# Optimization experiments

Measured on AMD Instinct MI355X. Metric: run time of the kernel, lower is better.

## Reference

```python
import jax, jax.numpy as jnp
import numpy as np

BN_EPS = 1e-3  # keras BatchNormalization default


def setup_inputs() -> dict:
    key = jax.random.key(0)
    ks = jax.random.split(key, 8)
    B, T, H, W, C = 2, 8, 28, 28, 256
    Ci = 128
    s_in = 1.0 / np.sqrt(C)
    s_ci = 1.0 / np.sqrt(Ci)
    return {
        "x": jax.random.normal(ks[0], (B, T, H, W, C), dtype=jnp.float32),
        "Wg": jax.random.normal(ks[1], (C, Ci), dtype=jnp.float32) * s_in,
        "bg": jnp.zeros((Ci,), dtype=jnp.float32),
        "Wt": jax.random.normal(ks[2], (C, Ci), dtype=jnp.float32) * s_in,
        "bt": jnp.zeros((Ci,), dtype=jnp.float32),
        "Wp": jax.random.normal(ks[3], (C, Ci), dtype=jnp.float32) * s_in,
        "bp": jnp.zeros((Ci,), dtype=jnp.float32),
        "Wo": jax.random.normal(ks[4], (Ci, C), dtype=jnp.float32) * s_ci,
        "bo": jnp.zeros((C,), dtype=jnp.float32),
        "gamma": jnp.ones((C,), dtype=jnp.float32),
        "beta": jnp.zeros((C,), dtype=jnp.float32),
        "moving_mean": jnp.zeros((C,), dtype=jnp.float32),
        "moving_var": jnp.ones((C,), dtype=jnp.float32),
    }


def reference(x, Wg, bg, Wt, bt, Wp, bp, Wo, bo, gamma, beta, moving_mean, moving_var):
    B, T, H, W, C = x.shape
    Ci = Wg.shape[1]
    N = T * H * W
    xf = x.reshape(B, N, C)  # flatten spatial-temporal positions
    # 1x1x1 convs are per-position channel GEMMs
    g_x = xf @ Wg + bg        # [B, N, Ci]
    theta_x = xf @ Wt + bt    # [B, N, Ci]
    phi_x = xf @ Wp + bp      # [B, N, Ci]
    # f = softmax(theta @ phi^T) -- unscaled single-head global attention
    f = jnp.einsum('bnc,bmc->bnm', theta_x, phi_x)  # [B, N, N]
    f = jax.nn.softmax(f, axis=-1)
    y = jnp.einsum('bnm,bmc->bnc', f, g_x)           # [B, N, Ci]
    # conv_out (1x1x1) back to C channels
    y = y @ Wo + bo                                   # [B, N, C]
    # BatchNorm, inference mode (training=None -> moving statistics)
    y = gamma * (y - moving_mean) * jax.lax.rsqrt(moving_var + BN_EPS) + beta
    return x + y.reshape(B, T, H, W, C)
```

## Files before the change

kernel.cpp:

```cpp
#include <hip/hip_runtime.h>

#define BB 2
#define NN 6272
#define CC 256
#define CI 128
#define SEG 7
#define KVSEG (NN / SEG)
#define NIT (KVSEG / 32)
#define LOG2E 1.44269504088896f
#define THR 12.0f

typedef _Float16 f16;
typedef __attribute__((ext_vector_type(2))) __fp16 fp16v2;
typedef __attribute__((ext_vector_type(8))) _Float16 f16x8;
typedef __attribute__((ext_vector_type(4))) float f32x4;

__global__ __launch_bounds__(256) void prep_kernel(
    const float* __restrict__ Wg, const float* __restrict__ Wt, const float* __restrict__ Wp,
    const float* __restrict__ Wo, const float* __restrict__ bg, const float* __restrict__ bt,
    const float* __restrict__ bp, const float* __restrict__ bo,
    const float* __restrict__ gamma, const float* __restrict__ beta,
    const float* __restrict__ mmean, const float* __restrict__ mvar,
    f16* __restrict__ WallT, f16* __restrict__ WoT,
    float* __restrict__ ball, float* __restrict__ bnsc, float* __restrict__ bnsh)
{
    const int idx = blockIdx.x * 256 + threadIdx.x;
    if (idx < 384*256) {
        const int j = idx >> 8, k = idx & 255;
        float v;
        if (j < 128)      v = Wg[k*CI + j];
        else if (j < 256) v = Wt[k*CI + (j-128)] * LOG2E;
        else              v = Wp[k*CI + (j-256)];
        WallT[j*256 + k] = (f16)v;
    } else if (idx < 384*256 + 256*128) {
        const int i2 = idx - 384*256;
        const int ci = i2 >> 7, k = i2 & 127;
        WoT[ci*CI + k] = (f16)Wo[k*CC + ci];
    } else {
        const int i3 = idx - (384*256 + 256*128);
        if (i3 < 384) {
            float v;
            if (i3 < 128)      v = bg[i3];
            else if (i3 < 256) v = bt[i3-128] * LOG2E;
            else               v = bp[i3-256];
            ball[i3] = v;
        } else if (i3 < 640) {
            const int c = i3 - 384;
            bnsc[c] = gamma[c] * rsqrtf(mvar[c] + 1e-3f);
        } else if (i3 < 896) {
            const int c = i3 - 640;
            float sc = gamma[c] * rsqrtf(mvar[c] + 1e-3f);
            bnsh[c] = beta[c] + sc * (bo[c] - mmean[c]);
        }
    }
}

__global__ __launch_bounds__(256) void proj_gemm(
    const float* __restrict__ x, const f16* __restrict__ WallT, const float* __restrict__ ball,
    f16* __restrict__ th, f16* __restrict__ ph, f16* __restrict__ gT)
{
    __shared__ __align__(16) f16 xls[32*264];
    __shared__ __align__(16) f16 gls[128*40];

    const int tid = threadIdx.x;
    const int wid = tid >> 6, lane = tid & 63;
    const int l15 = lane & 15, lg = lane >> 4;
    const int p0 = blockIdx.x * 32;

    {
        const int row = tid >> 3, c0 = (tid & 7) * 32;
        const float* xsrc = x + (size_t)(p0 + row) * CC + c0;
        f16 buf[32];
        #pragma unroll
        for (int i = 0; i < 8; ++i) {
            float4 v = *reinterpret_cast<const float4*>(xsrc + 4*i);
            buf[4*i+0]=(f16)v.x; buf[4*i+1]=(f16)v.y; buf[4*i+2]=(f16)v.z; buf[4*i+3]=(f16)v.w;
        }
        #pragma unroll
        for (int i = 0; i < 4; ++i)
            *reinterpret_cast<f16x8*>(&xls[row*264 + c0 + 8*i]) =
                *reinterpret_cast<f16x8*>(&buf[8*i]);
    }
    __syncthreads();

    f32x4 acc[2][6];
    #pragma unroll
    for (int pt = 0; pt < 2; ++pt)
        #pragma unroll
        for (int t = 0; t < 6; ++t) acc[pt][t] = (f32x4){0.f,0.f,0.f,0.f};

    const f16* wbase = WallT + (size_t)(wid*96 + l15)*256 + lg*8;
    for (int kk = 0; kk < 8; ++kk) {
        f16x8 a0 = *reinterpret_cast<const f16x8*>(&xls[l15*264 + kk*32 + lg*8]);
        f16x8 a1 = *reinterpret_cast<const f16x8*>(&xls[(16 + l15)*264 + kk*32 + lg*8]);
        #pragma unroll
        for (int t = 0; t < 6; ++t) {
            f16x8 bfr = *reinterpret_cast<const f16x8*>(wbase + (size_t)t*16*256 + kk*32);
            acc[0][t] = __builtin_amdgcn_mfma_f32_16x16x32_f16(a0, bfr, acc[0][t], 0, 0, 0);
            acc[1][t] = __builtin_amdgcn_mfma_f32_16x16x32_f16(a1, bfr, acc[1][t], 0, 0, 0);
        }
    }

    const int bidx = (p0 >= NN) ? 1 : 0;
    const int n0 = p0 - bidx * NN;

    #pragma unroll
    for (int t = 0; t < 6; ++t) {
        const int j0 = wid*96 + t*16;
        const float bv = ball[j0 + l15];
        if (j0 < 128) {
            #pragma unroll
            for (int pt = 0; pt < 2; ++pt)
                #pragma unroll
                for (int r = 0; r < 4; ++r)
                    gls[(j0 + l15)*40 + pt*16 + lg*4 + r] = (f16)(acc[pt][t][r] + bv);
        } else if (j0 < 256) {
            #pragma unroll
            for (int pt = 0; pt < 2; ++pt) {
                f16* dst = th + (size_t)(p0 + pt*16 + lg*4)*CI + (j0 - 128) + l15;
                #pragma unroll
                for (int r = 0; r < 4; ++r)
                    dst[(size_t)r*CI] = (f16)(acc[pt][t][r] + bv);
            }
        } else {
            #pragma unroll
            for (int pt = 0; pt < 2; ++pt) {
                f16* dst = ph + (size_t)(p0 + pt*16 + lg*4)*CI + (j0 - 256) + l15;
                #pragma unroll
                for (int r = 0; r < 4; ++r)
                    dst[(size_t)r*CI] = (f16)(acc[pt][t][r] + bv);
            }
        }
    }
    __syncthreads();
    {
        const int ci = tid >> 1, half = tid & 1;
        f16x8 v0 = *reinterpret_cast<const f16x8*>(&gls[ci*40 + half*16]);
        f16x8 v1 = *reinterpret_cast<const f16x8*>(&gls[ci*40 + half*16 + 8]);
        f16* gdst = gT + ((size_t)bidx*(NN/32) + (n0 >> 5))*(CI*32) + ci*32 + half*16;
        *reinterpret_cast<f16x8*>(gdst)     = v0;
        *reinterpret_cast<f16x8*>(gdst + 8) = v1;
    }
}

__global__ __launch_bounds__(256, 3) void attn_kernel(
    const f16* __restrict__ th, const f16* __restrict__ ph,
    const f16* __restrict__ gT, f16* __restrict__ pacc, float* __restrict__ pml)
{
    __shared__ __align__(16) f16 ph_lds[32 * 128];
    __shared__ __align__(16) f16 g_lds[128 * 32];
    __shared__ __align__(16) f16 pT_lds[4][2][16][40];

    const int b   = blockIdx.z;
    const int seg = blockIdx.y;
    const int tid = threadIdx.x;
    const int wid = tid >> 6;
    const int lane = tid & 63;
    const int l15 = lane & 15;
    const int lg  = lane >> 4;
    const int qw  = blockIdx.x * 128 + wid * 32;

    const f16* thb = th + (size_t)b * NN * CI;
    const f16* phb = ph + (size_t)b * NN * CI;
    const f16* gTb = gT + (size_t)b * (NN/32) * (CI*32);

    f16x8 bf[2][4];
    #pragma unroll
    for (int qt = 0; qt < 2; ++qt) {
        const f16* trow = thb + (size_t)(qw + qt*16 + l15) * CI + lg * 8;
        #pragma unroll
        for (int kk = 0; kk < 4; ++kk)
            bf[qt][kk] = *reinterpret_cast<const f16x8*>(trow + kk * 32);
    }

    f32x4 acc[2][8];
    f32x4 accl[2];
    float m[2] = {-INFINITY, -INFINITY};
    #pragma unroll
    for (int qt = 0; qt < 2; ++qt) {
        #pragma unroll
        for (int ct = 0; ct < 8; ++ct) acc[qt][ct] = (f32x4){0.f,0.f,0.f,0.f};
        accl[qt] = (f32x4){0.f,0.f,0.f,0.f};
    }

    const f16x8 onesA = {(f16)1,(f16)1,(f16)1,(f16)1,(f16)1,(f16)1,(f16)1,(f16)1};

    const int prow = tid >> 3, pcol = (tid & 7) * 16;
    const int pswz = (prow & 7) << 3;
    const int pc0 = pcol ^ pswz, pc1 = (pcol + 8) ^ pswz;
    const int grow = tid >> 1, gcs = (tid & 1) * 16;
    const int gswz = ((grow >> 1) & 3) << 3;
    const int gc0 = gcs ^ gswz, gc1 = (gcs + 8) ^ gswz;

    const int kv_base = seg * KVSEG;
    const int t0 = kv_base >> 5;
    const int xsw = (l15 & 7) << 3;

    #pragma unroll 1
    for (int it = 0; it < NIT; ++it) {
        const int kv0 = kv_base + it * 32;

        const f16* ps = phb + (size_t)(kv0 + prow) * CI + pcol;
        f16x8 pv0 = *reinterpret_cast<const f16x8*>(ps);
        f16x8 pv1 = *reinterpret_cast<const f16x8*>(ps + 8);
        const f16* gs = gTb + (size_t)(t0 + it) * (CI*32) + tid * 16;
        f16x8 gv0 = *reinterpret_cast<const f16x8*>(gs);
        f16x8 gv1 = *reinterpret_cast<const f16x8*>(gs + 8);

        __syncthreads();
        *reinterpret_cast<f16x8*>(&ph_lds[prow*128 + pc0]) = pv0;
        *reinterpret_cast<f16x8*>(&ph_lds[prow*128 + pc1]) = pv1;
        *reinterpret_cast<f16x8*>(&g_lds[grow*32 + gc0])   = gv0;
        *reinterpret_cast<f16x8*>(&g_lds[grow*32 + gc1])   = gv1;
        __syncthreads();

        f32x4 s00 = (f32x4){0.f,0.f,0.f,0.f}, s01 = (f32x4){0.f,0.f,0.f,0.f};
        f32x4 s10 = (f32x4){0.f,0.f,0.f,0.f}, s11 = (f32x4){0.f,0.f,0.f,0.f};
        #pragma unroll
        for (int kk = 0; kk < 4; ++kk) {
            const int coff = (kk*32 + lg*8) ^ xsw;
            f16x8 a0 = *reinterpret_cast<const f16x8*>(&ph_lds[l15*128 + coff]);
            f16x8 a1 = *reinterpret_cast<const f16x8*>(&ph_lds[(16 + l15)*128 + coff]);
            s00 = __builtin_amdgcn_mfma_f32_16x16x32_f16(a0, bf[0][kk], s00, 0, 0, 0);
            s01 = __builtin_amdgcn_mfma_f32_16x16x32_f16(a1, bf[0][kk], s01, 0, 0, 0);
            s10 = __builtin_amdgcn_mfma_f32_16x16x32_f16(a0, bf[1][kk], s10, 0, 0, 0);
            s11 = __builtin_amdgcn_mfma_f32_16x16x32_f16(a1, bf[1][kk], s11, 0, 0, 0);
        }

        float tm0 = fmaxf(fmaxf(fmaxf(s00[0], s00[1]), fmaxf(s00[2], s00[3])),
                          fmaxf(fmaxf(s01[0], s01[1]), fmaxf(s01[2], s01[3])));
        float tm1 = fmaxf(fmaxf(fmaxf(s10[0], s10[1]), fmaxf(s10[2], s10[3])),
                          fmaxf(fmaxf(s11[0], s11[1]), fmaxf(s11[2], s11[3])));
        tm0 = fmaxf(tm0, __shfl_xor(tm0, 16));
        tm0 = fmaxf(tm0, __shfl_xor(tm0, 32));
        tm1 = fmaxf(tm1, __shfl_xor(tm1, 16));
        tm1 = fmaxf(tm1, __shfl_xor(tm1, 32));
        if (__any((tm0 > m[0] + THR) || (tm1 > m[1] + THR))) {
            float nm0 = fmaxf(m[0], tm0), nm1 = fmaxf(m[1], tm1);
            float sc0 = __builtin_amdgcn_exp2f(m[0] - nm0);
            float sc1 = __builtin_amdgcn_exp2f(m[1] - nm1);
            m[0] = nm0; m[1] = nm1;
            #pragma unroll
            for (int ct = 0; ct < 8; ++ct) {
                acc[0][ct][0] *= sc0; acc[0][ct][1] *= sc0; acc[0][ct][2] *= sc0; acc[0][ct][3] *= sc0;
                acc[1][ct][0] *= sc1; acc[1][ct][1] *= sc1; acc[1][ct][2] *= sc1; acc[1][ct][3] *= sc1;
            }
            accl[0][0] *= sc0; accl[0][1] *= sc0; accl[0][2] *= sc0; accl[0][3] *= sc0;
            accl[1][0] *= sc1; accl[1][1] *= sc1; accl[1][2] *= sc1; accl[1][3] *= sc1;
        }

        {
            union { fp16v2 h[2]; float2 f; } u0, u1;
            u0.h[0] = __builtin_amdgcn_cvt_pkrtz(__builtin_amdgcn_exp2f(s00[0] - m[0]),
                                                 __builtin_amdgcn_exp2f(s00[1] - m[0]));
            u0.h[1] = __builtin_amdgcn_cvt_pkrtz(__builtin_amdgcn_exp2f(s00[2] - m[0]),
                                                 __builtin_amdgcn_exp2f(s00[3] - m[0]));
            u1.h[0] = __builtin_amdgcn_cvt_pkrtz(__builtin_amdgcn_exp2f(s01[0] - m[0]),
                                                 __builtin_amdgcn_exp2f(s01[1] - m[0]));
            u1.h[1] = __builtin_amdgcn_cvt_pkrtz(__builtin_amdgcn_exp2f(s01[2] - m[0]),
                                                 __builtin_amdgcn_exp2f(s01[3] - m[0]));
            *reinterpret_cast<float2*>(&pT_lds[wid][0][l15][4*lg])      = u0.f;
            *reinterpret_cast<float2*>(&pT_lds[wid][0][l15][16 + 4*lg]) = u1.f;
            u0.h[0] = __builtin_amdgcn_cvt_pkrtz(__builtin_amdgcn_exp2f(s10[0] - m[1]),
                                                 __builtin_amdgcn_exp2f(s10[1] - m[1]));
            u0.h[1] = __builtin_amdgcn_cvt_pkrtz(__builtin_amdgcn_exp2f(s10[2] - m[1]),
                                                 __builtin_amdgcn_exp2f(s10[3] - m[1]));
            u1.h[0] = __builtin_amdgcn_cvt_pkrtz(__builtin_amdgcn_exp2f(s11[0] - m[1]),
                                                 __builtin_amdgcn_exp2f(s11[1] - m[1]));
            u1.h[1] = __builtin_amdgcn_cvt_pkrtz(__builtin_amdgcn_exp2f(s11[2] - m[1]),
                                                 __builtin_amdgcn_exp2f(s11[3] - m[1]));
            *reinterpret_cast<float2*>(&pT_lds[wid][1][l15][4*lg])      = u0.f;
            *reinterpret_cast<float2*>(&pT_lds[wid][1][l15][16 + 4*lg]) = u1.f;
        }
        asm volatile("s_waitcnt lgkmcnt(0)" ::: "memory");
        f16x8 pa0 = *reinterpret_cast<const f16x8*>(&pT_lds[wid][0][l15][8*lg]);
        f16x8 pa1 = *reinterpret_cast<const f16x8*>(&pT_lds[wid][1][l15][8*lg]);

        const int grsw = ((l15 >> 1) & 3) << 3;
        #pragma unroll
        for (int ct = 0; ct < 8; ++ct) {
            f16x8 ga = *reinterpret_cast<const f16x8*>(&g_lds[(ct*16 + l15)*32 + (lg*8 ^ grsw)]);
            acc[0][ct] = __builtin_amdgcn_mfma_f32_16x16x32_f16(ga, pa0, acc[0][ct], 0, 0, 0);
            acc[1][ct] = __builtin_amdgcn_mfma_f32_16x16x32_f16(ga, pa1, acc[1][ct], 0, 0, 0);
        }
        accl[0] = __builtin_amdgcn_mfma_f32_16x16x32_f16(onesA, pa0, accl[0], 0, 0, 0);
        accl[1] = __builtin_amdgcn_mfma_f32_16x16x32_f16(onesA, pa1, accl[1], 0, 0, 0);
    }

    const float inv[2] = {1.0f / accl[0][0], 1.0f / accl[1][0]};
    #pragma unroll
    for (int qt = 0; qt < 2; ++qt) {
        f16* pb = pacc + (size_t)(b*SEG + seg) * CI * NN + qw + qt*16 + l15;
        #pragma unroll
        for (int ct = 0; ct < 8; ++ct)
            #pragma unroll
            for (int r = 0; r < 4; ++r)
                pb[(size_t)(ct*16 + lg*4 + r) * NN] = (f16)(acc[qt][ct][r] * inv[qt]);
    }

    if (lg == 0) {
        #pragma unroll
        for (int qt = 0; qt < 2; ++qt) {
            float* mlb = pml + ((size_t)(b*SEG + seg) * NN + qw + qt*16 + l15) * 2;
            mlb[0] = m[qt];
            mlb[1] = accl[qt][0];
        }
    }
}

__global__ __launch_bounds__(256) void out_gemm(
    const float* __restrict__ x, const f16* __restrict__ pacc, const float* __restrict__ pml,
    const f16* __restrict__ WoT, const float* __restrict__ bnsc, const float* __restrict__ bnsh,
    float* __restrict__ out)
{
    __shared__ __align__(16) f16 yls[32*136];
    __shared__ float wl_lds[SEG][32];

    const int tid = threadIdx.x;
    const int p0 = blockIdx.x * 32;
    const int bidx = (p0 >= NN) ? 1 : 0;
    const int n0 = p0 - bidx * NN;

    if (tid < 32) {
        const int q = n0 + tid;
        float mv[SEG], lv[SEG];
        #pragma unroll
        for (int s = 0; s < SEG; ++s) {
            const float* p = pml + ((size_t)(bidx*SEG + s) * NN + q) * 2;
            mv[s] = p[0];
            lv[s] = p[1];
        }
        float M = mv[0];
        #pragma unroll
        for (int s = 1; s < SEG; ++s) M = fmaxf(M, mv[s]);
        float wl[SEG], wsum = 0.f;
        #pragma unroll
        for (int s = 0; s < SEG; ++s) {
            wl[s] = __builtin_amdgcn_exp2f(mv[s] - M) * lv[s];
            wsum += wl[s];
        }
        const float inv = 1.0f / wsum;
        #pragma unroll
        for (int s = 0; s < SEG; ++s) wl_lds[s][tid] = wl[s] * inv;
    }
    __syncthreads();

    {
        const int ci = tid >> 1, pbase = (tid & 1) * 16;
        float o[16];
        #pragma unroll
        for (int i = 0; i < 16; ++i) o[i] = 0.f;
        for (int s = 0; s < SEG; ++s) {
            const f16* pb = pacc + ((size_t)(bidx*SEG + s) * CI + ci) * NN + n0 + pbase;
            f16x8 v0 = *reinterpret_cast<const f16x8*>(pb);
            f16x8 v1 = *reinterpret_cast<const f16x8*>(pb + 8);
            #pragma unroll
            for (int i = 0; i < 8; ++i) {
                o[i]     = fmaf(wl_lds[s][pbase + i],     (float)v0[i], o[i]);
                o[8 + i] = fmaf(wl_lds[s][pbase + 8 + i], (float)v1[i], o[8 + i]);
            }
        }
        #pragma unroll
        for (int i = 0; i < 16; ++i)
            yls[(pbase + i)*136 + ci] = (f16)o[i];
    }
    __syncthreads();

    const int wid = tid >> 6, lane = tid & 63;
    const int l15 = lane & 15, lg = lane >> 4;

    f32x4 acc[2][4];
    #pragma unroll
    for (int pt = 0; pt < 2; ++pt)
        #pragma unroll
        for (int t = 0; t < 4; ++t) acc[pt][t] = (f32x4){0.f,0.f,0.f,0.f};

    const f16* wb = WoT + (size_t)(wid*64 + l15)*CI + lg*8;
    #pragma unroll
    for (int kk = 0; kk < 4; ++kk) {
        f16x8 a0 = *reinterpret_cast<const f16x8*>(&yls[l15*136 + kk*32 + lg*8]);
        f16x8 a1 = *reinterpret_cast<const f16x8*>(&yls[(16 + l15)*136 + kk*32 + lg*8]);
        #pragma unroll
        for (int t = 0; t < 4; ++t) {
            f16x8 bfr = *reinterpret_cast<const f16x8*>(wb + (size_t)t*16*CI + kk*32);
            acc[0][t] = __builtin_amdgcn_mfma_f32_16x16x32_f16(a0, bfr, acc[0][t], 0, 0, 0);
            acc[1][t] = __builtin_amdgcn_mfma_f32_16x16x32_f16(a1, bfr, acc[1][t], 0, 0, 0);
        }
    }

    #pragma unroll
    for (int t = 0; t < 4; ++t) {
        const int ci = wid*64 + t*16 + l15;
        const float sc = bnsc[ci], sh = bnsh[ci];
        #pragma unroll
        for (int pt = 0; pt < 2; ++pt)
            #pragma unroll
            for (int r = 0; r < 4; ++r) {
                const size_t idx = (size_t)(p0 + pt*16 + lg*4 + r)*CC + ci;
                out[idx] = x[idx] + fmaf(sc, acc[pt][t][r], sh);
            }
    }
}

extern "C" void kernel_launch(void* const* d_in, const int* in_sizes, int n_in,
                              void* d_out, int out_size, void* d_ws, size_t ws_size,
                              hipStream_t stream)
{
    const float* x     = (const float*)d_in[0];
    const float* Wg    = (const float*)d_in[1];
    const float* bg    = (const float*)d_in[2];
    const float* Wt    = (const float*)d_in[3];
    const float* bt    = (const float*)d_in[4];
    const float* Wp    = (const float*)d_in[5];
    const float* bp    = (const float*)d_in[6];
    const float* Wo    = (const float*)d_in[7];
    const float* bo    = (const float*)d_in[8];
    const float* gamma = (const float*)d_in[9];
    const float* beta  = (const float*)d_in[10];
    const float* mmean = (const float*)d_in[11];
    const float* mvar  = (const float*)d_in[12];
    float* out = (float*)d_out;

    const size_t PB = (size_t)BB * NN * CI;
    f16*   th   = (f16*)d_ws;
    f16*   ph   = th + PB;
    f16*   gT   = ph + PB;
    f16*   pacc = gT + PB;
    float* pml  = (float*)(pacc + (size_t)BB * SEG * NN * CI);
    f16*   WallT= (f16*)(pml + (size_t)BB * SEG * NN * 2);
    f16*   WoT  = WallT + 384*256;
    float* ball = (float*)(WoT + 256*CI);
    float* bnsc = ball + 384;
    float* bnsh = bnsc + 256;

    prep_kernel<<<516, 256, 0, stream>>>(Wg, Wt, Wp, Wo, bg, bt, bp, bo,
                                         gamma, beta, mmean, mvar,
                                         WallT, WoT, ball, bnsc, bnsh);
    proj_gemm<<<BB * NN / 32, 256, 0, stream>>>(x, WallT, ball, th, ph, gT);
    attn_kernel<<<dim3(NN / 128, SEG, BB), 256, 0, stream>>>(th, ph, gT, pacc, pml);
    out_gemm<<<BB * NN / 32, 256, 0, stream>>>(x, pacc, pml, WoT, bnsc, bnsh, out);
}
```

Measured before the change: 96.69 us.

## Double attention KV tile to 64 keys per iteration with new LDS swizzles

The flash-attention loop now processes 64 key/value rows per iteration instead of 32. This halves the number of barrier pairs, max/rescale checks and loop overheads per segment, and issues more MFMAs between synchronisations. LDS tiles and their XOR swizzles are reworked for the wider tiles. Launch bounds drop from 3 to 2 blocks per CU to fit the extra LDS and registers, which lowers occupancy and latency hiding.

```diff
diff --git a/kernel.cpp b/kernel.cpp
--- a/kernel.cpp
+++ b/kernel.cpp
@@ -6,7 +6,8 @@
 #define CI 128
 #define SEG 7
 #define KVSEG (NN / SEG)
-#define NIT (KVSEG / 32)
+#define KVB 64
+#define NIT (KVSEG / KVB)
 #define LOG2E 1.44269504088896f
 #define THR 12.0f
 
@@ -143,13 +144,13 @@
     }
 }
 
-__global__ __launch_bounds__(256, 3) void attn_kernel(
+__global__ __launch_bounds__(256, 2) void attn_kernel(
     const f16* __restrict__ th, const f16* __restrict__ ph,
     const f16* __restrict__ gT, f16* __restrict__ pacc, float* __restrict__ pml)
 {
-    __shared__ __align__(16) f16 ph_lds[32 * 128];
-    __shared__ __align__(16) f16 g_lds[128 * 32];
-    __shared__ __align__(16) f16 pT_lds[4][2][16][40];
+    __shared__ __align__(16) f16 ph_lds[64 * 128];
+    __shared__ __align__(16) f16 g_lds[128 * 64];
+    __shared__ __align__(16) f16 pT_lds[4][2][16][72];
 
     const int b   = blockIdx.z;
     const int seg = blockIdx.y;
@@ -185,52 +186,69 @@
 
     const f16x8 onesA = {(f16)1,(f16)1,(f16)1,(f16)1,(f16)1,(f16)1,(f16)1,(f16)1};
 
-    const int prow = tid >> 3, pcol = (tid & 7) * 16;
-    const int pswz = (prow & 7) << 3;
-    const int pc0 = pcol ^ pswz, pc1 = (pcol + 8) ^ pswz;
+    const int prow = tid >> 2, pcol = (tid & 3) * 32;
+    const int pX = ((prow >> 1) & 7) << 3;
     const int grow = tid >> 1, gcs = (tid & 1) * 16;
-    const int gswz = ((grow >> 1) & 3) << 3;
-    const int gc0 = gcs ^ gswz, gc1 = (gcs + 8) ^ gswz;
+    const int gtw = (grow >> 2) & 3;
+    const int gX = (gtw & 1) * 32 + (gtw >> 1) * 8;
+    const int xswr = ((l15 >> 1) & 7) << 3;
+    const int gtr = (l15 >> 2) & 3;
+    const int grX = (gtr & 1) * 32 + (gtr >> 1) * 8;
 
     const int kv_base = seg * KVSEG;
     const int t0 = kv_base >> 5;
-    const int xsw = (l15 & 7) << 3;
 
     #pragma unroll 1
     for (int it = 0; it < NIT; ++it) {
-        const int kv0 = kv_base + it * 32;
+        const int kv0 = kv_base + it * KVB;
 
         const f16* ps = phb + (size_t)(kv0 + prow) * CI + pcol;
         f16x8 pv0 = *reinterpret_cast<const f16x8*>(ps);
         f16x8 pv1 = *reinterpret_cast<const f16x8*>(ps + 8);
-        const f16* gs = gTb + (size_t)(t0 + it) * (CI*32) + tid * 16;
-        f16x8 gv0 = *reinterpret_cast<const f16x8*>(gs);
-        f16x8 gv1 = *reinterpret_cast<const f16x8*>(gs + 8);
+        f16x8 pv2 = *reinterpret_cast<const f16x8*>(ps + 16);
+        f16x8 pv3 = *reinterpret_cast<const f16x8*>(ps + 24);
+        const f16* gsA = gTb + (size_t)(t0 + 2*it) * (CI*32) + grow*32 + gcs;
+        const f16* gsB = gsA + CI*32;
+        f16x8 gva0 = *reinterpret_cast<const f16x8*>(gsA);
+        f16x8 gva1 = *reinterpret_cast<const f16x8*>(gsA + 8);
+        f16x8 gvb0 = *reinterpret_cast<const f16x8*>(gsB);
+        f16x8 gvb1 = *reinterpret_cast<const f16x8*>(gsB + 8);
 
         __syncthreads();
-        *reinterpret_cast<f16x8*>(&ph_lds[prow*128 + pc0]) = pv0;
-        *reinterpret_cast<f16x8*>(&ph_lds[prow*128 + pc1]) = pv1;
-        *reinterpret_cast<f16x8*>(&g_lds[grow*32 + gc0])   = gv0;
-        *reinterpret_cast<f16x8*>(&g_lds[grow*32 + gc1])   = gv1;
+        *reinterpret_cast<f16x8*>(&ph_lds[prow*128 + ((pcol     ) ^ pX)]) = pv0;
+        *reinterpret_cast<f16x8*>(&ph_lds[prow*128 + ((pcol +  8) ^ pX)]) = pv1;
+        *reinterpret_cast<f16x8*>(&ph_lds[prow*128 + ((pcol + 16) ^ pX)]) = pv2;
+        *reinterpret_cast<f16x8*>(&ph_lds[prow*128 + ((pcol + 24) ^ pX)]) = pv3;
+        *reinterpret_cast<f16x8*>(&g_lds[grow*64 + ((gcs     ) ^ gX)]) = gva0;
+        *reinterpret_cast<f16x8*>(&g_lds[grow*64 + ((gcs +  8) ^ gX)]) = gva1;
+        *reinterpret_cast<f16x8*>(&g_lds[grow*64 + ((gcs + 32) ^ gX)]) = gvb0;
+        *reinterpret_cast<f16x8*>(&g_lds[grow*64 + ((gcs + 40) ^ gX)]) = gvb1;
         __syncthreads();
 
-        f32x4 s00 = (f32x4){0.f,0.f,0.f,0.f}, s01 = (f32x4){0.f,0.f,0.f,0.f};
-        f32x4 s10 = (f32x4){0.f,0.f,0.f,0.f}, s11 = (f32x4){0.f,0.f,0.f,0.f};
+        f32x4 s[2][4];
+        #pragma unroll
+        for (int qt = 0; qt < 2; ++qt)
+            #pragma unroll
+            for (int kvt = 0; kvt < 4; ++kvt) s[qt][kvt] = (f32x4){0.f,0.f,0.f,0.f};
         #pragma unroll
         for (int kk = 0; kk < 4; ++kk) {
-            const int coff = (kk*32 + lg*8) ^ xsw;
-            f16x8 a0 = *reinterpret_cast<const f16x8*>(&ph_lds[l15*128 + coff]);
-            f16x8 a1 = *reinterpret_cast<const f16x8*>(&ph_lds[(16 + l15)*128 + coff]);
-            s00 = __builtin_amdgcn_mfma_f32_16x16x32_f16(a0, bf[0][kk], s00, 0, 0, 0);
-            s01 = __builtin_amdgcn_mfma_f32_16x16x32_f16(a1, bf[0][kk], s01, 0, 0, 0);
-            s10 = __builtin_amdgcn_mfma_f32_16x16x32_f16(a0, bf[1][kk], s10, 0, 0, 0);
-            s11 = __builtin_amdgcn_mfma_f32_16x16x32_f16(a1, bf[1][kk], s11, 0, 0, 0);
-        }
-
-        float tm0 = fmaxf(fmaxf(fmaxf(s00[0], s00[1]), fmaxf(s00[2], s00[3])),
-                          fmaxf(fmaxf(s01[0], s01[1]), fmaxf(s01[2], s01[3])));
-        float tm1 = fmaxf(fmaxf(fmaxf(s10[0], s10[1]), fmaxf(s10[2], s10[3])),
-                          fmaxf(fmaxf(s11[0], s11[1]), fmaxf(s11[2], s11[3])));
+            const int coff = (kk*32 + lg*8) ^ xswr;
+            #pragma unroll
+            for (int kvt = 0; kvt < 4; ++kvt) {
+                f16x8 a = *reinterpret_cast<const f16x8*>(&ph_lds[(kvt*16 + l15)*128 + coff]);
+                s[0][kvt] = __builtin_amdgcn_mfma_f32_16x16x32_f16(a, bf[0][kk], s[0][kvt], 0, 0, 0);
+                s[1][kvt] = __builtin_amdgcn_mfma_f32_16x16x32_f16(a, bf[1][kk], s[1][kvt], 0, 0, 0);
+            }
+        }
+
+        float tm0 = -1e30f, tm1 = -1e30f;
+        #pragma unroll
+        for (int kvt = 0; kvt < 4; ++kvt)
+            #pragma unroll
+            for (int r = 0; r < 4; ++r) {
+                tm0 = fmaxf(tm0, s[0][kvt][r]);
+                tm1 = fmaxf(tm1, s[1][kvt][r]);
+            }
         tm0 = fmaxf(tm0, __shfl_xor(tm0, 16));
         tm0 = fmaxf(tm0, __shfl_xor(tm0, 32));
         tm1 = fmaxf(tm1, __shfl_xor(tm1, 16));
@@ -249,42 +267,39 @@
             accl[1][0] *= sc1; accl[1][1] *= sc1; accl[1][2] *= sc1; accl[1][3] *= sc1;
         }
 
-        {
-            union { fp16v2 h[2]; float2 f; } u0, u1;
-            u0.h[0] = __builtin_amdgcn_cvt_pkrtz(__builtin_amdgcn_exp2f(s00[0] - m[0]),
-                                                 __builtin_amdgcn_exp2f(s00[1] - m[0]));
-            u0.h[1] = __builtin_amdgcn_cvt_pkrtz(__builtin_amdgcn_exp2f(s00[2] - m[0]),
-                                                 __builtin_amdgcn_exp2f(s00[3] - m[0]));
-            u1.h[0] = __builtin_amdgcn_cvt_pkrtz(__builtin_amdgcn_exp2f(s01[0] - m[0]),
-                                                 __builtin_amdgcn_exp2f(s01[1] - m[0]));
-            u1.h[1] = __builtin_amdgcn_cvt_pkrtz(__builtin_amdgcn_exp2f(s01[2] - m[0]),
-                                                 __builtin_amdgcn_exp2f(s01[3] - m[0]));
-            *reinterpret_cast<float2*>(&pT_lds[wid][0][l15][4*lg])      = u0.f;
-            *reinterpret_cast<float2*>(&pT_lds[wid][0][l15][16 + 4*lg]) = u1.f;
-            u0.h[0] = __builtin_amdgcn_cvt_pkrtz(__builtin_amdgcn_exp2f(s10[0] - m[1]),
-                                                 __builtin_amdgcn_exp2f(s10[1] - m[1]));
-            u0.h[1] = __builtin_amdgcn_cvt_pkrtz(__builtin_amdgcn_exp2f(s10[2] - m[1]),
-                                                 __builtin_amdgcn_exp2f(s10[3] - m[1]));
-            u1.h[0] = __builtin_amdgcn_cvt_pkrtz(__builtin_amdgcn_exp2f(s11[0] - m[1]),
-                                                 __builtin_amdgcn_exp2f(s11[1] - m[1]));
-            u1.h[1] = __builtin_amdgcn_cvt_pkrtz(__builtin_amdgcn_exp2f(s11[2] - m[1]),
-                                                 __builtin_amdgcn_exp2f(s11[3] - m[1]));
-            *reinterpret_cast<float2*>(&pT_lds[wid][1][l15][4*lg])      = u0.f;
-            *reinterpret_cast<float2*>(&pT_lds[wid][1][l15][16 + 4*lg]) = u1.f;
+        #pragma unroll
+        for (int qt = 0; qt < 2; ++qt) {
+            const float mq = m[qt];
+            #pragma unroll
+            for (int kvt = 0; kvt < 4; ++kvt) {
+                union { fp16v2 h[2]; float2 f; } u;
+                u.h[0] = __builtin_amdgcn_cvt_pkrtz(__builtin_amdgcn_exp2f(s[qt][kvt][0] - mq),
+                                                    __builtin_amdgcn_exp2f(s[qt][kvt][1] - mq));
+                u.h[1] = __builtin_amdgcn_cvt_pkrtz(__builtin_amdgcn_exp2f(s[qt][kvt][2] - mq),
+                                                    __builtin_amdgcn_exp2f(s[qt][kvt][3] - mq));
+                *reinterpret_cast<float2*>(&pT_lds[wid][qt][l15][kvt*16 + 4*lg]) = u.f;
+            }
         }
         asm volatile("s_waitcnt lgkmcnt(0)" ::: "memory");
-        f16x8 pa0 = *reinterpret_cast<const f16x8*>(&pT_lds[wid][0][l15][8*lg]);
-        f16x8 pa1 = *reinterpret_cast<const f16x8*>(&pT_lds[wid][1][l15][8*lg]);
-
-        const int grsw = ((l15 >> 1) & 3) << 3;
+        f16x8 pa00 = *reinterpret_cast<const f16x8*>(&pT_lds[wid][0][l15][8*lg]);
+        f16x8 pa01 = *reinterpret_cast<const f16x8*>(&pT_lds[wid][0][l15][32 + 8*lg]);
+        f16x8 pa10 = *reinterpret_cast<const f16x8*>(&pT_lds[wid][1][l15][8*lg]);
+        f16x8 pa11 = *reinterpret_cast<const f16x8*>(&pT_lds[wid][1][l15][32 + 8*lg]);
+
         #pragma unroll
         for (int ct = 0; ct < 8; ++ct) {
-            f16x8 ga = *reinterpret_cast<const f16x8*>(&g_lds[(ct*16 + l15)*32 + (lg*8 ^ grsw)]);
-            acc[0][ct] = __builtin_amdgcn_mfma_f32_16x16x32_f16(ga, pa0, acc[0][ct], 0, 0, 0);
-            acc[1][ct] = __builtin_amdgcn_mfma_f32_16x16x32_f16(ga, pa1, acc[1][ct], 0, 0, 0);
-        }
-        accl[0] = __builtin_amdgcn_mfma_f32_16x16x32_f16(onesA, pa0, accl[0], 0, 0, 0);
-        accl[1] = __builtin_amdgcn_mfma_f32_16x16x32_f16(onesA, pa1, accl[1], 0, 0, 0);
+            const f16* gr = &g_lds[(ct*16 + l15)*64];
+            f16x8 g0 = *reinterpret_cast<const f16x8*>(&gr[(lg*8) ^ grX]);
+            f16x8 g1 = *reinterpret_cast<const f16x8*>(&gr[(32 + lg*8) ^ grX]);
+            acc[0][ct] = __builtin_amdgcn_mfma_f32_16x16x32_f16(g0, pa00, acc[0][ct], 0, 0, 0);
+            acc[0][ct] = __builtin_amdgcn_mfma_f32_16x16x32_f16(g1, pa01, acc[0][ct], 0, 0, 0);
+            acc[1][ct] = __builtin_amdgcn_mfma_f32_16x16x32_f16(g0, pa10, acc[1][ct], 0, 0, 0);
+            acc[1][ct] = __builtin_amdgcn_mfma_f32_16x16x32_f16(g1, pa11, acc[1][ct], 0, 0, 0);
+        }
+        accl[0] = __builtin_amdgcn_mfma_f32_16x16x32_f16(onesA, pa00, accl[0], 0, 0, 0);
+        accl[0] = __builtin_amdgcn_mfma_f32_16x16x32_f16(onesA, pa01, accl[0], 0, 0, 0);
+        accl[1] = __builtin_amdgcn_mfma_f32_16x16x32_f16(onesA, pa10, accl[1], 0, 0, 0);
+        accl[1] = __builtin_amdgcn_mfma_f32_16x16x32_f16(onesA, pa11, accl[1], 0, 0, 0);
     }
 
     const float inv[2] = {1.0f / accl[0][0], 1.0f / accl[1][0]};
```

After: 115.6 us. 1.2x slower.
